# Kernel optimization log

Measured on AMD Instinct MI355X. Metric: run time of the kernel, lower is better.

The kernel has to match this reference:

```python
import jax, jax.numpy as jnp
import numpy as np

B, T, C = 4, 2048, 1024
H = 16
D = C // H  # head_dim = 64


def setup_inputs() -> dict:
    key = jax.random.key(0)
    k1, k2, k3 = jax.random.split(key, 3)
    x = jax.random.normal(k1, (B, T, C), dtype=jnp.float32)
    # torch Linear weights are [out_features, in_features]; scale like default init
    W_qkv = jax.random.normal(k2, (3 * C, C), dtype=jnp.float32) * (1.0 / np.sqrt(C))
    W_proj = jax.random.normal(k3, (C, C), dtype=jnp.float32) * (1.0 / np.sqrt(C))
    return {"x": x, "W_qkv": W_qkv, "W_proj": W_proj}


def reference(x, W_qkv, W_proj):
    # qkv projection: x @ W_qkv.T -> (B,T,3C), split into q,k,v
    qkv = jnp.einsum('btc,oc->bto', x, W_qkv)
    q, k, v = jnp.split(qkv, 3, axis=-1)
    # reshape to (B,H,T,D)
    q = q.reshape(B, T, H, D).transpose(0, 2, 1, 3)
    k = k.reshape(B, T, H, D).transpose(0, 2, 1, 3)
    v = v.reshape(B, T, H, D).transpose(0, 2, 1, 3)
    scale = jnp.sqrt(jnp.float32(D))
    # explicit (B,H,T,T) scores, as in the original module
    attn = jnp.einsum('bhqd,bhkd->bhqk', q, k) / scale
    causal = jnp.tril(jnp.ones((T, T), dtype=bool))
    attn = jnp.where(causal, attn, -jnp.inf)
    attn = jax.nn.softmax(attn, axis=-1)
    out = jnp.einsum('bhqk,bhkd->bhqd', attn, v)
    out = out.transpose(0, 2, 1, 3).reshape(B, T, C)
    return jnp.einsum('btc,oc->bto', out, W_proj)
```

## Files before the change

kernel.cpp:

```cpp
#include <hip/hip_runtime.h>

typedef __attribute__((ext_vector_type(8))) short short8;
typedef __attribute__((ext_vector_type(4))) float f32x4;
typedef __attribute__((ext_vector_type(16))) float f32x16;
typedef __attribute__((ext_vector_type(4))) unsigned int u32x4;

#define AS1(p) ((const __attribute__((address_space(1))) void*)(p))
#define AS3(p) ((__attribute__((address_space(3))) void*)(p))

#define B_ 4
#define T_ 2048
#define C_ 1024
#define H_ 16
#define D_ 64
#define M_ (B_*T_)

#define MFIX 16.0f

__device__ __forceinline__ unsigned short f2bf(float f) {
  union { float f; unsigned u; } v; v.f = f;
  return (unsigned short)((v.u + 0x7fffu + ((v.u >> 16) & 1u)) >> 16);
}

__device__ __forceinline__ unsigned cvt_pk_bf16(float lo, float hi2) {
  unsigned r;
  asm("v_cvt_pk_bf16_f32 %0, %1, %2" : "=v"(r) : "v"(lo), "v"(hi2));
  return r;
}

__device__ __forceinline__ float exp2_fast(float x) {
  return __builtin_amdgcn_exp2f(x);
}

__global__ void cast_f32_bf16(const float* __restrict__ in, unsigned short* __restrict__ out, int n) {
  int i = (blockIdx.x * blockDim.x + threadIdx.x) * 4;
  int stride = gridDim.x * blockDim.x * 4;
  for (; i < n; i += stride) {
    float4 f = *reinterpret_cast<const float4*>(in + i);
    ushort4 o;
    o.x = f2bf(f.x); o.y = f2bf(f.y); o.z = f2bf(f.z); o.w = f2bf(f.w);
    *reinterpret_cast<ushort4*>(out + i) = o;
  }
}

__global__ __launch_bounds__(512, 2) void gemm256_qkv(
    const unsigned short* __restrict__ A, const unsigned short* __restrict__ Bt,
    int M, int N, int K,
    unsigned short* __restrict__ qb, unsigned short* __restrict__ kb,
    unsigned short* __restrict__ vtb) {
  __shared__ unsigned short Ls[2][2][2][128 * 64];
  const int tid = threadIdx.x;
  const int lane = tid & 63;
  const int wid = tid >> 6;
  const int wm = wid >> 2;
  const int wn = wid & 3;
  const int lr = lane & 15, lg = lane >> 4;
  const int ntb_cnt = N >> 8;
  const int nwg = gridDim.x;
  const int cpx = nwg >> 3;
  const int wg = (blockIdx.x & 7) * cpx + (blockIdx.x >> 3);
  const int mt = wg / ntb_cnt, ntb = wg % ntb_cnt;
  const int m0 = mt << 8, n0 = ntb << 8;

  f32x4 acc[8][4];
  #pragma unroll
  for (int i = 0; i < 8; i++)
    #pragma unroll
    for (int j = 0; j < 4; j++) acc[i][j] = (f32x4){0.f, 0.f, 0.f, 0.f};

  const int wbase16 = (tid & ~63) * 16;

  auto stage = [&](int buf, int mat, int half, int k0) {
    const unsigned short* srcbase = (mat == 0) ? (A  + (size_t)(m0 + half * 128) * K)
                                               : (Bt + (size_t)(n0 + half * 128) * K);
    char* ldsbase = (char*)&Ls[buf][mat][half][0];
    #pragma unroll
    for (int i = 0; i < 2; i++) {
      int s = i * 512 + tid;
      int row = s >> 3;
      int src = ((s & 7) * 16) ^ ((row & 7) << 4);
      const unsigned short* g = srcbase + (size_t)row * K + k0 + (src >> 1);
      char* l = ldsbase + i * 8192 + wbase16;
      __builtin_amdgcn_global_load_lds(AS1(g), AS3(l), 16, 0, 0);
    }
  };

  const int ktiles = K >> 6;
  stage(0, 0, 0, 0); stage(0, 0, 1, 0); stage(0, 1, 0, 0); stage(0, 1, 1, 0);

  for (int t = 0; t < ktiles; ++t) {
    const int cur = t & 1;
    const int nk0 = (t + 1) << 6;
    const bool more = (t + 1 < ktiles);
    short8 bfrag[4][2];

    #pragma unroll
    for (int p = 0; p < 4; p++) {
      if (more) stage(cur ^ 1, p >> 1, p & 1, nk0);
      if (p == 0) {
        if (more) asm volatile("s_waitcnt vmcnt(2)" ::: "memory");
        else      asm volatile("s_waitcnt vmcnt(0)" ::: "memory");
      }
      __builtin_amdgcn_sched_barrier(0);
      __builtin_amdgcn_s_barrier();
      __builtin_amdgcn_sched_barrier(0);

      if (p == 0) {
        #pragma unroll
        for (int ni = 0; ni < 4; ni++)
          #pragma unroll
          for (int ks = 0; ks < 2; ks++) {
            const int rih = (wn & 1) * 64 + ni * 16 + lr;
            bfrag[ni][ks] = *reinterpret_cast<const short8*>(
                (const char*)&Ls[cur][1][wn >> 1][0] + rih * 128 +
                ((ks * 64 + lg * 16) ^ ((lr & 7) << 4)));
          }
      }
      short8 af[2][2];
      #pragma unroll
      for (int m2 = 0; m2 < 2; m2++)
        #pragma unroll
        for (int ks = 0; ks < 2; ks++) {
          const int rih = (2 * p + m2) * 16 + lr;
          af[m2][ks] = *reinterpret_cast<const short8*>(
              (const char*)&Ls[cur][0][wm][0] + rih * 128 +
              ((ks * 64 + lg * 16) ^ ((lr & 7) << 4)));
        }

      __builtin_amdgcn_s_setprio(1);
      #pragma unroll
      for (int m2 = 0; m2 < 2; m2++)
        #pragma unroll
        for (int ni = 0; ni < 4; ni++)
          #pragma unroll
          for (int ks = 0; ks < 2; ks++)
            acc[2 * p + m2][ni] = __builtin_amdgcn_mfma_f32_16x16x32_bf16(
                af[m2][ks], bfrag[ni][ks], acc[2 * p + m2][ni], 0, 0, 0);
      __builtin_amdgcn_s_setprio(0);
      __builtin_amdgcn_sched_barrier(0);
      __builtin_amdgcn_s_barrier();
    }
  }

  #pragma unroll
  for (int mi = 0; mi < 8; mi++) {
    #pragma unroll
    for (int ni = 0; ni < 4; ni++) {
      #pragma unroll
      for (int r = 0; r < 4; r++) {
        int row = m0 + wm * 128 + mi * 16 + lg * 4 + r;
        int col = n0 + wn * 64 + ni * 16 + lr;
        float v = acc[mi][ni][r];
        int which = col >> 10;
        int c = col & 1023;
        int h = c >> 6, d = c & 63;
        int b = row >> 11, t2 = row & 2047;
        if (which == 0) {
          qb[(((size_t)(b * H_ + h)) * T_ + t2) * D_ + d] = f2bf(v * 0.18033688f);
        } else if (which == 1) {
          kb[(((size_t)(b * H_ + h)) * T_ + t2) * D_ + d] = f2bf(v);
        } else {
          vtb[(((size_t)(b * H_ + h)) * D_ + d) * T_ + t2] = f2bf(v);
        }
      }
    }
  }
}

__global__ __launch_bounds__(256) void gemm_bt(
    const unsigned short* __restrict__ A, const unsigned short* __restrict__ Bt,
    float* __restrict__ Cout, int M, int N, int K) {
  __shared__ unsigned short As[2][128 * 32];
  __shared__ unsigned short Bs[2][128 * 32];
  const int tid = threadIdx.x;
  const int lane = tid & 63;
  const int w = tid >> 6;
  const int wr = w >> 1, wc = w & 1;
  const int lr = lane & 15, lg = lane >> 4;
  const int ntiles = N >> 7;
  const int nwg = gridDim.x;
  const int cpx = nwg >> 3;
  const int wg = (blockIdx.x & 7) * cpx + (blockIdx.x >> 3);
  const int mt = wg / ntiles, nt = wg % ntiles;
  const int m0 = mt << 7, n0 = nt << 7;

  f32x4 acc[4][4];
  #pragma unroll
  for (int i = 0; i < 4; i++)
    #pragma unroll
    for (int j = 0; j < 4; j++) acc[i][j] = (f32x4){0.f, 0.f, 0.f, 0.f};

  const int wbase = tid & ~63;

  auto stage = [&](int buf, int k0) {
    #pragma unroll
    for (int t = 0; t < 2; t++) {
      int slot = t * 256 + tid;
      int row = slot >> 2, kg = slot & 3;
      const unsigned short* ga = A + (size_t)(m0 + row) * K + k0 + kg * 8;
      char* la = (char*)As[buf] + (size_t)(t * 256 + wbase) * 16;
      __builtin_amdgcn_global_load_lds(AS1(ga), AS3(la), 16, 0, 0);
      const unsigned short* gb = Bt + (size_t)(n0 + row) * K + k0 + kg * 8;
      char* lb = (char*)Bs[buf] + (size_t)(t * 256 + wbase) * 16;
      __builtin_amdgcn_global_load_lds(AS1(gb), AS3(lb), 16, 0, 0);
    }
  };

  const int nIter = K >> 5;
  stage(0, 0);
  __syncthreads();

  for (int it = 0; it < nIter; ++it) {
    const int cur = it & 1;
    if (it + 1 < nIter) stage(cur ^ 1, (it + 1) << 5);

    short8 af[4], bf[4];
    #pragma unroll
    for (int i = 0; i < 4; i++) {
      af[i] = *reinterpret_cast<const short8*>(&As[cur][(wr * 64 + i * 16 + lr) * 32 + lg * 8]);
      bf[i] = *reinterpret_cast<const short8*>(&Bs[cur][(wc * 64 + i * 16 + lr) * 32 + lg * 8]);
    }
    #pragma unroll
    for (int i = 0; i < 4; i++)
      #pragma unroll
      for (int j = 0; j < 4; j++)
        acc[i][j] = __builtin_amdgcn_mfma_f32_16x16x32_bf16(af[i], bf[j], acc[i][j], 0, 0, 0);

    __syncthreads();
  }

  #pragma unroll
  for (int i = 0; i < 4; i++)
    #pragma unroll
    for (int j = 0; j < 4; j++)
      #pragma unroll
      for (int r = 0; r < 4; r++) {
        int row = m0 + wr * 64 + i * 16 + lg * 4 + r;
        int col = n0 + wc * 64 + j * 16 + lr;
        Cout[(size_t)row * N + col] = acc[i][j][r];
      }
}

__global__ __launch_bounds__(128, 2) void attn_fwd(
    const unsigned short* __restrict__ qb, const unsigned short* __restrict__ kb,
    const unsigned short* __restrict__ vtb, unsigned short* __restrict__ ob) {
  __shared__ unsigned short Kl[2 * 64 * 64];
  const int tid = threadIdx.x;
  const int lane = tid & 63;
  const int w = tid >> 6;
  const int q31 = lane & 31;
  const int hi = lane >> 5;

  const int bid = blockIdx.x;
  const int bh = (bid & 7) * 8 + ((bid >> 3) & 7);
  const int qt = 15 - (bid >> 6);
  const int qb0 = qt << 7;
  const int b = bh >> 4, h = bh & 15;

  const unsigned short* Q  = qb  + (size_t)bh * T_ * D_;
  const unsigned short* Kp = kb  + (size_t)bh * T_ * D_;
  const unsigned short* Vt = vtb + (size_t)bh * D_ * T_;

  const int qloA = qb0 + w * 64;
  const int qloB = qloA + 32;
  const int qgA = qloA + q31;
  const int qgB = qloB + q31;

  short8 qfA[4], qfB[4];
  #pragma unroll
  for (int ch = 0; ch < 4; ch++) {
    qfA[ch] = *reinterpret_cast<const short8*>(Q + qgA * D_ + ch * 16 + hi * 8);
    qfB[ch] = *reinterpret_cast<const short8*>(Q + qgB * D_ + ch * 16 + hi * 8);
  }

  f32x16 accA0, accA1, accB0, accB1;
  #pragma unroll
  for (int r = 0; r < 16; r++) { accA0[r] = 0.f; accA1[r] = 0.f; accB0[r] = 0.f; accB1[r] = 0.f; }
  float lA = 0.f, lB = 0.f;

  auto stage = [&](int buf, int k0) {
    #pragma unroll
    for (int sh = 0; sh < 4; sh++) {
      int s = sh * 128 + tid;
      int row = s >> 3;
      int xlin = (s & 7) * 16;
      int src = xlin ^ ((row & 7) << 4);
      const unsigned short* g = Kp + (k0 + row) * D_ + (src >> 1);
      char* l = (char*)Kl + buf * 8192 + (size_t)(sh * 128 + (tid & ~63)) * 16;
      __builtin_amdgcn_global_load_lds(AS1(g), AS3(l), 16, 0, 0);
    }
  };

  const int nt = qb0 / 64 + 2;
  stage(0, 0);
  __syncthreads();

  for (int t = 0; t < nt; t++) {
    const int k0 = t * 64;
    if (t + 1 < nt) stage((t + 1) & 1, k0 + 64);

    if (k0 <= qloA + 63) {
      short8 vf[2][4];
      #pragma unroll
      for (int ds = 0; ds < 2; ds++)
        #pragma unroll
        for (int kk = 0; kk < 4; kk++)
          vf[ds][kk] = *reinterpret_cast<const short8*>(
              Vt + (ds * 32 + q31) * T_ + k0 + kk * 16 + hi * 8);
      __builtin_amdgcn_sched_barrier(0);

      const char* kbase = (const char*)Kl + (t & 1) * 8192;

      f32x16 sA0, sA1, sB0, sB1;
      #pragma unroll
      for (int r = 0; r < 16; r++) { sA0[r] = 0.f; sA1[r] = 0.f; sB0[r] = 0.f; sB1[r] = 0.f; }
      __builtin_amdgcn_s_setprio(1);
      #pragma unroll
      for (int kc = 0; kc < 2; kc++) {
        const int row = kc * 32 + q31;
        const int sw = (row & 7) << 4;
        #pragma unroll
        for (int ch = 0; ch < 4; ch++) {
          short8 kf = *reinterpret_cast<const short8*>(kbase + row * 128 + ((ch * 32 + hi * 16) ^ sw));
          if (kc == 0) {
            sA0 = __builtin_amdgcn_mfma_f32_32x32x16_bf16(kf, qfA[ch], sA0, 0, 0, 0);
            sB0 = __builtin_amdgcn_mfma_f32_32x32x16_bf16(kf, qfB[ch], sB0, 0, 0, 0);
          } else {
            sA1 = __builtin_amdgcn_mfma_f32_32x32x16_bf16(kf, qfA[ch], sA1, 0, 0, 0);
            sB1 = __builtin_amdgcn_mfma_f32_32x32x16_bf16(kf, qfB[ch], sB1, 0, 0, 0);
          }
        }
      }
      __builtin_amdgcn_s_setprio(0);

      if (k0 + 63 > qloA) {
        #pragma unroll
        for (int r = 0; r < 16; r++) {
          const int kl = (r & 3) + 8 * (r >> 2) + 4 * hi;
          if (k0 + kl > qgA)      sA0[r] = -INFINITY;
          if (k0 + 32 + kl > qgA) sA1[r] = -INFINITY;
        }
      }
      if (k0 + 63 > qloB) {
        #pragma unroll
        for (int r = 0; r < 16; r++) {
          const int kl = (r & 3) + 8 * (r >> 2) + 4 * hi;
          if (k0 + kl > qgB)      sB0[r] = -INFINITY;
          if (k0 + 32 + kl > qgB) sB1[r] = -INFINITY;
        }
      }

      #pragma unroll
      for (int r = 0; r < 16; r++) {
        sA0[r] = exp2_fast(sA0[r] - MFIX); sA1[r] = exp2_fast(sA1[r] - MFIX);
        sB0[r] = exp2_fast(sB0[r] - MFIX); sB1[r] = exp2_fast(sB1[r] - MFIX);
      }
      {
        float tsA[8], tsB[8];
        #pragma unroll
        for (int r = 0; r < 8; r++) {
          tsA[r] = (sA0[r] + sA0[r + 8]) + (sA1[r] + sA1[r + 8]);
          tsB[r] = (sB0[r] + sB0[r + 8]) + (sB1[r] + sB1[r + 8]);
        }
        #pragma unroll
        for (int off = 4; off > 0; off >>= 1)
          #pragma unroll
          for (int r = 0; r < off; r++) { tsA[r] += tsA[r + off]; tsB[r] += tsB[r + off]; }
        lA += tsA[0];
        lB += tsB[0];
      }

      #pragma unroll
      for (int kc = 0; kc < 2; kc++) {
        unsigned w8A[8], rw8A[8], w8B[8], rw8B[8];
        #pragma unroll
        for (int j = 0; j < 8; j++) {
          float aA  = (kc == 0) ? sA0[2 * j] : sA1[2 * j];
          float bA  = (kc == 0) ? sA0[2 * j + 1] : sA1[2 * j + 1];
          w8A[j] = cvt_pk_bf16(aA, bA);
          float aB  = (kc == 0) ? sB0[2 * j] : sB1[2 * j];
          float bB  = (kc == 0) ? sB0[2 * j + 1] : sB1[2 * j + 1];
          w8B[j] = cvt_pk_bf16(aB, bB);
        }
        #pragma unroll
        for (int j = 0; j < 8; j++) {
          rw8A[j] = (unsigned)__shfl_xor((int)w8A[j], 32);
          rw8B[j] = (unsigned)__shfl_xor((int)w8B[j], 32);
        }

        __builtin_amdgcn_s_setprio(1);
        #pragma unroll
        for (int ks = 0; ks < 2; ks++) {
          unsigned a0 = hi ? rw8A[4 * ks + 2] : w8A[4 * ks + 0];
          unsigned a1 = hi ? rw8A[4 * ks + 3] : w8A[4 * ks + 1];
          unsigned a2 = hi ? w8A[4 * ks + 2]  : rw8A[4 * ks + 0];
          unsigned a3 = hi ? w8A[4 * ks + 3]  : rw8A[4 * ks + 1];
          u32x4 pwA = {a0, a1, a2, a3};
          unsigned b0 = hi ? rw8B[4 * ks + 2] : w8B[4 * ks + 0];
          unsigned b1 = hi ? rw8B[4 * ks + 3] : w8B[4 * ks + 1];
          unsigned b2 = hi ? w8B[4 * ks + 2]  : rw8B[4 * ks + 0];
          unsigned b3 = hi ? w8B[4 * ks + 3]  : rw8B[4 * ks + 1];
          u32x4 pwB = {b0, b1, b2, b3};
          union { u32x4 u; short8 s; } cvA, cvB;
          cvA.u = pwA; cvB.u = pwB;
          const int kk = kc * 2 + ks;
          #pragma unroll
          for (int ds = 0; ds < 2; ds++) {
            if (ds == 0) {
              accA0 = __builtin_amdgcn_mfma_f32_32x32x16_bf16(vf[0][kk], cvA.s, accA0, 0, 0, 0);
              accB0 = __builtin_amdgcn_mfma_f32_32x32x16_bf16(vf[0][kk], cvB.s, accB0, 0, 0, 0);
            } else {
              accA1 = __builtin_amdgcn_mfma_f32_32x32x16_bf16(vf[1][kk], cvA.s, accA1, 0, 0, 0);
              accB1 = __builtin_amdgcn_mfma_f32_32x32x16_bf16(vf[1][kk], cvB.s, accB1, 0, 0, 0);
            }
          }
        }
        __builtin_amdgcn_s_setprio(0);
      }
    }
    __syncthreads();
  }

  lA += __shfl_xor(lA, 32);
  lB += __shfl_xor(lB, 32);

  {
    const float invA = 1.f / lA;
    unsigned short* orow = ob + ((size_t)(b * T_ + qgA)) * C_ + h * D_;
    #pragma unroll
    for (int ds = 0; ds < 2; ds++) {
      #pragma unroll
      for (int g = 0; g < 4; g++) {
        ushort4 o4;
        if (ds == 0) {
          o4.x = f2bf(accA0[4 * g + 0] * invA); o4.y = f2bf(accA0[4 * g + 1] * invA);
          o4.z = f2bf(accA0[4 * g + 2] * invA); o4.w = f2bf(accA0[4 * g + 3] * invA);
        } else {
          o4.x = f2bf(accA1[4 * g + 0] * invA); o4.y = f2bf(accA1[4 * g + 1] * invA);
          o4.z = f2bf(accA1[4 * g + 2] * invA); o4.w = f2bf(accA1[4 * g + 3] * invA);
        }
        *reinterpret_cast<ushort4*>(orow + ds * 32 + 8 * g + 4 * hi) = o4;
      }
    }
  }
  {
    const float invB = 1.f / lB;
    unsigned short* orow = ob + ((size_t)(b * T_ + qgB)) * C_ + h * D_;
    #pragma unroll
    for (int ds = 0; ds < 2; ds++) {
      #pragma unroll
      for (int g = 0; g < 4; g++) {
        ushort4 o4;
        if (ds == 0) {
          o4.x = f2bf(accB0[4 * g + 0] * invB); o4.y = f2bf(accB0[4 * g + 1] * invB);
          o4.z = f2bf(accB0[4 * g + 2] * invB); o4.w = f2bf(accB0[4 * g + 3] * invB);
        } else {
          o4.x = f2bf(accB1[4 * g + 0] * invB); o4.y = f2bf(accB1[4 * g + 1] * invB);
          o4.z = f2bf(accB1[4 * g + 2] * invB); o4.w = f2bf(accB1[4 * g + 3] * invB);
        }
        *reinterpret_cast<ushort4*>(orow + ds * 32 + 8 * g + 4 * hi) = o4;
      }
    }
  }
}

extern "C" void kernel_launch(void* const* d_in, const int* in_sizes, int n_in,
                              void* d_out, int out_size, void* d_ws, size_t ws_size,
                              hipStream_t stream) {
  const float* x = (const float*)d_in[0];
  const float* W_qkv = (const float*)d_in[1];
  const float* W_proj = (const float*)d_in[2];
  float* out = (float*)d_out;

  char* ws = (char*)d_ws;
  unsigned short* xb     = (unsigned short*)(ws);
  unsigned short* wqkvb  = (unsigned short*)(ws + 16777216);
  unsigned short* wprojb = (unsigned short*)(ws + 23068672);
  unsigned short* qb     = (unsigned short*)(ws + 25165824);
  unsigned short* kb     = (unsigned short*)(ws + 41943040);
  unsigned short* vtb    = (unsigned short*)(ws + 58720256);
  unsigned short* ob     = xb;

  const int nx = M_ * C_;
  const int nwqkv = 3 * C_ * C_;
  const int nwproj = C_ * C_;

  cast_f32_bf16<<<2048, 256, 0, stream>>>(x, xb, nx);
  cast_f32_bf16<<<2048, 256, 0, stream>>>(W_qkv, wqkvb, nwqkv);
  cast_f32_bf16<<<1024, 256, 0, stream>>>(W_proj, wprojb, nwproj);

  gemm256_qkv<<<(M_ / 256) * (3 * C_ / 256), 512, 0, stream>>>(
      xb, wqkvb, M_, 3 * C_, C_, qb, kb, vtb);

  attn_fwd<<<B_ * H_ * (T_ / 128), 128, 0, stream>>>(qb, kb, vtb, ob);

  gemm_bt<<<(M_ / 128) * (C_ / 128), 256, 0, stream>>>(
      ob, wprojb, out, M_, C_, C_);
}
```

Measured before the change: 205.2 us.

## Split attention into single-wave blocks of 64 query rows with waitcnt-based pipelining

The attention kernel now launches one 64-thread wavefront per 64-row query tile, doubling the grid and removing the two-wave block. With a single wave, __syncthreads is replaced by explicit s_waitcnt vmcnt on the async K-to-LDS staging, and the per-wave causal skip branch is dropped because every tile iterates only up to its diagonal. This removes block-level barriers and the idle tail of the second wave, at the cost of K tiles no longer being shared across two waves through LDS. Occupancy also changes through the launch bounds and per-block LDS use.

```diff
diff --git a/kernel.cpp b/kernel.cpp
--- a/kernel.cpp
+++ b/kernel.cpp
@@ -241,30 +241,26 @@
       }
 }
 
-__global__ __launch_bounds__(128, 2) void attn_fwd(
+__global__ __launch_bounds__(64, 1) void attn_fwd(
     const unsigned short* __restrict__ qb, const unsigned short* __restrict__ kb,
     const unsigned short* __restrict__ vtb, unsigned short* __restrict__ ob) {
   __shared__ unsigned short Kl[2 * 64 * 64];
-  const int tid = threadIdx.x;
-  const int lane = tid & 63;
-  const int w = tid >> 6;
+  const int lane = threadIdx.x;
   const int q31 = lane & 31;
   const int hi = lane >> 5;
 
   const int bid = blockIdx.x;
   const int bh = (bid & 7) * 8 + ((bid >> 3) & 7);
-  const int qt = 15 - (bid >> 6);
-  const int qb0 = qt << 7;
+  const int qt = 31 - (bid >> 6);
+  const int qb0 = qt << 6;
   const int b = bh >> 4, h = bh & 15;
 
   const unsigned short* Q  = qb  + (size_t)bh * T_ * D_;
   const unsigned short* Kp = kb  + (size_t)bh * T_ * D_;
   const unsigned short* Vt = vtb + (size_t)bh * D_ * T_;
 
-  const int qloA = qb0 + w * 64;
-  const int qloB = qloA + 32;
-  const int qgA = qloA + q31;
-  const int qgB = qloB + q31;
+  const int qgA = qb0 + q31;
+  const int qgB = qb0 + 32 + q31;
 
   short8 qfA[4], qfB[4];
   #pragma unroll
@@ -280,145 +276,140 @@
 
   auto stage = [&](int buf, int k0) {
     #pragma unroll
-    for (int sh = 0; sh < 4; sh++) {
-      int s = sh * 128 + tid;
+    for (int sh = 0; sh < 8; sh++) {
+      int s = sh * 64 + lane;
       int row = s >> 3;
-      int xlin = (s & 7) * 16;
-      int src = xlin ^ ((row & 7) << 4);
+      int src = ((s & 7) * 16) ^ ((row & 7) << 4);
       const unsigned short* g = Kp + (k0 + row) * D_ + (src >> 1);
-      char* l = (char*)Kl + buf * 8192 + (size_t)(sh * 128 + (tid & ~63)) * 16;
+      char* l = (char*)Kl + buf * 8192 + sh * 1024;
       __builtin_amdgcn_global_load_lds(AS1(g), AS3(l), 16, 0, 0);
     }
   };
 
-  const int nt = qb0 / 64 + 2;
+  const int nt = qt + 1;
   stage(0, 0);
-  __syncthreads();
 
   for (int t = 0; t < nt; t++) {
     const int k0 = t * 64;
-    if (t + 1 < nt) stage((t + 1) & 1, k0 + 64);
-
-    if (k0 <= qloA + 63) {
-      short8 vf[2][4];
-      #pragma unroll
-      for (int ds = 0; ds < 2; ds++)
+    if (t + 1 < nt) {
+      stage((t + 1) & 1, k0 + 64);
+      asm volatile("s_waitcnt vmcnt(8)" ::: "memory");
+    } else {
+      asm volatile("s_waitcnt vmcnt(0)" ::: "memory");
+    }
+    __builtin_amdgcn_sched_barrier(0);
+
+    short8 vf[2][4];
+    #pragma unroll
+    for (int ds = 0; ds < 2; ds++)
+      #pragma unroll
+      for (int kk = 0; kk < 4; kk++)
+        vf[ds][kk] = *reinterpret_cast<const short8*>(
+            Vt + (ds * 32 + q31) * T_ + k0 + kk * 16 + hi * 8);
+    __builtin_amdgcn_sched_barrier(0);
+
+    const char* kbase = (const char*)Kl + (t & 1) * 8192;
+
+    f32x16 sA0, sA1, sB0, sB1;
+    #pragma unroll
+    for (int r = 0; r < 16; r++) { sA0[r] = 0.f; sA1[r] = 0.f; sB0[r] = 0.f; sB1[r] = 0.f; }
+    __builtin_amdgcn_s_setprio(1);
+    #pragma unroll
+    for (int kc = 0; kc < 2; kc++) {
+      const int row = kc * 32 + q31;
+      const int sw = (row & 7) << 4;
+      #pragma unroll
+      for (int ch = 0; ch < 4; ch++) {
+        short8 kf = *reinterpret_cast<const short8*>(kbase + row * 128 + ((ch * 32 + hi * 16) ^ sw));
+        if (kc == 0) {
+          sA0 = __builtin_amdgcn_mfma_f32_32x32x16_bf16(kf, qfA[ch], sA0, 0, 0, 0);
+          sB0 = __builtin_amdgcn_mfma_f32_32x32x16_bf16(kf, qfB[ch], sB0, 0, 0, 0);
+        } else {
+          sA1 = __builtin_amdgcn_mfma_f32_32x32x16_bf16(kf, qfA[ch], sA1, 0, 0, 0);
+          sB1 = __builtin_amdgcn_mfma_f32_32x32x16_bf16(kf, qfB[ch], sB1, 0, 0, 0);
+        }
+      }
+    }
+    __builtin_amdgcn_s_setprio(0);
+
+    if (t == nt - 1) {
+      #pragma unroll
+      for (int r = 0; r < 16; r++) {
+        const int kl = (r & 3) + 8 * (r >> 2) + 4 * hi;
+        if (k0 + kl > qgA)      sA0[r] = -INFINITY;
+        if (k0 + 32 + kl > qgA) sA1[r] = -INFINITY;
+        if (k0 + kl > qgB)      sB0[r] = -INFINITY;
+        if (k0 + 32 + kl > qgB) sB1[r] = -INFINITY;
+      }
+    }
+
+    #pragma unroll
+    for (int r = 0; r < 16; r++) {
+      sA0[r] = exp2_fast(sA0[r] - MFIX); sA1[r] = exp2_fast(sA1[r] - MFIX);
+      sB0[r] = exp2_fast(sB0[r] - MFIX); sB1[r] = exp2_fast(sB1[r] - MFIX);
+    }
+    {
+      float tsA[8], tsB[8];
+      #pragma unroll
+      for (int r = 0; r < 8; r++) {
+        tsA[r] = (sA0[r] + sA0[r + 8]) + (sA1[r] + sA1[r + 8]);
+        tsB[r] = (sB0[r] + sB0[r + 8]) + (sB1[r] + sB1[r + 8]);
+      }
+      #pragma unroll
+      for (int off = 4; off > 0; off >>= 1)
         #pragma unroll
-        for (int kk = 0; kk < 4; kk++)
-          vf[ds][kk] = *reinterpret_cast<const short8*>(
-              Vt + (ds * 32 + q31) * T_ + k0 + kk * 16 + hi * 8);
-      __builtin_amdgcn_sched_barrier(0);
-
-      const char* kbase = (const char*)Kl + (t & 1) * 8192;
-
-      f32x16 sA0, sA1, sB0, sB1;
-      #pragma unroll
-      for (int r = 0; r < 16; r++) { sA0[r] = 0.f; sA1[r] = 0.f; sB0[r] = 0.f; sB1[r] = 0.f; }
+        for (int r = 0; r < off; r++) { tsA[r] += tsA[r + off]; tsB[r] += tsB[r + off]; }
+      lA += tsA[0];
+      lB += tsB[0];
+    }
+
+    #pragma unroll
+    for (int kc = 0; kc < 2; kc++) {
+      unsigned w8A[8], rw8A[8], w8B[8], rw8B[8];
+      #pragma unroll
+      for (int j = 0; j < 8; j++) {
+        float aA  = (kc == 0) ? sA0[2 * j] : sA1[2 * j];
+        float bA  = (kc == 0) ? sA0[2 * j + 1] : sA1[2 * j + 1];
+        w8A[j] = cvt_pk_bf16(aA, bA);
+        float aB  = (kc == 0) ? sB0[2 * j] : sB1[2 * j];
+        float bB  = (kc == 0) ? sB0[2 * j + 1] : sB1[2 * j + 1];
+        w8B[j] = cvt_pk_bf16(aB, bB);
+      }
+      #pragma unroll
+      for (int j = 0; j < 8; j++) {
+        rw8A[j] = (unsigned)__shfl_xor((int)w8A[j], 32);
+        rw8B[j] = (unsigned)__shfl_xor((int)w8B[j], 32);
+      }
+
       __builtin_amdgcn_s_setprio(1);
       #pragma unroll
-      for (int kc = 0; kc < 2; kc++) {
-        const int row = kc * 32 + q31;
-        const int sw = (row & 7) << 4;
+      for (int ks = 0; ks < 2; ks++) {
+        unsigned a0 = hi ? rw8A[4 * ks + 2] : w8A[4 * ks + 0];
+        unsigned a1 = hi ? rw8A[4 * ks + 3] : w8A[4 * ks + 1];
+        unsigned a2 = hi ? w8A[4 * ks + 2]  : rw8A[4 * ks + 0];
+        unsigned a3 = hi ? w8A[4 * ks + 3]  : rw8A[4 * ks + 1];
+        u32x4 pwA = {a0, a1, a2, a3};
+        unsigned b0 = hi ? rw8B[4 * ks + 2] : w8B[4 * ks + 0];
+        unsigned b1 = hi ? rw8B[4 * ks + 3] : w8B[4 * ks + 1];
+        unsigned b2 = hi ? w8B[4 * ks + 2]  : rw8B[4 * ks + 0];
+        unsigned b3 = hi ? w8B[4 * ks + 3]  : rw8B[4 * ks + 1];
+        u32x4 pwB = {b0, b1, b2, b3};
+        union { u32x4 u; short8 s; } cvA, cvB;
+        cvA.u = pwA; cvB.u = pwB;
+        const int kk = kc * 2 + ks;
         #pragma unroll
-        for (int ch = 0; ch < 4; ch++) {
-          short8 kf = *reinterpret_cast<const short8*>(kbase + row * 128 + ((ch * 32 + hi * 16) ^ sw));
-          if (kc == 0) {
-            sA0 = __builtin_amdgcn_mfma_f32_32x32x16_bf16(kf, qfA[ch], sA0, 0, 0, 0);
-            sB0 = __builtin_amdgcn_mfma_f32_32x32x16_bf16(kf, qfB[ch], sB0, 0, 0, 0);
+        for (int ds = 0; ds < 2; ds++) {
+          if (ds == 0) {
+            accA0 = __builtin_amdgcn_mfma_f32_32x32x16_bf16(vf[0][kk], cvA.s, accA0, 0, 0, 0);
+            accB0 = __builtin_amdgcn_mfma_f32_32x32x16_bf16(vf[0][kk], cvB.s, accB0, 0, 0, 0);
           } else {
-            sA1 = __builtin_amdgcn_mfma_f32_32x32x16_bf16(kf, qfA[ch], sA1, 0, 0, 0);
-            sB1 = __builtin_amdgcn_mfma_f32_32x32x16_bf16(kf, qfB[ch], sB1, 0, 0, 0);
+            accA1 = __builtin_amdgcn_mfma_f32_32x32x16_bf16(vf[1][kk], cvA.s, accA1, 0, 0, 0);
+            accB1 = __builtin_amdgcn_mfma_f32_32x32x16_bf16(vf[1][kk], cvB.s, accB1, 0, 0, 0);
           }
         }
       }
       __builtin_amdgcn_s_setprio(0);
-
-      if (k0 + 63 > qloA) {
-        #pragma unroll
-        for (int r = 0; r < 16; r++) {
-          const int kl = (r & 3) + 8 * (r >> 2) + 4 * hi;
-          if (k0 + kl > qgA)      sA0[r] = -INFINITY;
-          if (k0 + 32 + kl > qgA) sA1[r] = -INFINITY;
-        }
-      }
-      if (k0 + 63 > qloB) {
-        #pragma unroll
-        for (int r = 0; r < 16; r++) {
-          const int kl = (r & 3) + 8 * (r >> 2) + 4 * hi;
-          if (k0 + kl > qgB)      sB0[r] = -INFINITY;
-          if (k0 + 32 + kl > qgB) sB1[r] = -INFINITY;
-        }
-      }
-
-      #pragma unroll
-      for (int r = 0; r < 16; r++) {
-        sA0[r] = exp2_fast(sA0[r] - MFIX); sA1[r] = exp2_fast(sA1[r] - MFIX);
-        sB0[r] = exp2_fast(sB0[r] - MFIX); sB1[r] = exp2_fast(sB1[r] - MFIX);
-      }
-      {
-        float tsA[8], tsB[8];
-        #pragma unroll
-        for (int r = 0; r < 8; r++) {
-          tsA[r] = (sA0[r] + sA0[r + 8]) + (sA1[r] + sA1[r + 8]);
-          tsB[r] = (sB0[r] + sB0[r + 8]) + (sB1[r] + sB1[r + 8]);
-        }
-        #pragma unroll
-        for (int off = 4; off > 0; off >>= 1)
-          #pragma unroll
-          for (int r = 0; r < off; r++) { tsA[r] += tsA[r + off]; tsB[r] += tsB[r + off]; }
-        lA += tsA[0];
-        lB += tsB[0];
-      }
-
-      #pragma unroll
-      for (int kc = 0; kc < 2; kc++) {
-        unsigned w8A[8], rw8A[8], w8B[8], rw8B[8];
-        #pragma unroll
-        for (int j = 0; j < 8; j++) {
-          float aA  = (kc == 0) ? sA0[2 * j] : sA1[2 * j];
-          float bA  = (kc == 0) ? sA0[2 * j + 1] : sA1[2 * j + 1];
-          w8A[j] = cvt_pk_bf16(aA, bA);
-          float aB  = (kc == 0) ? sB0[2 * j] : sB1[2 * j];
-          float bB  = (kc == 0) ? sB0[2 * j + 1] : sB1[2 * j + 1];
-          w8B[j] = cvt_pk_bf16(aB, bB);
-        }
-        #pragma unroll
-        for (int j = 0; j < 8; j++) {
-          rw8A[j] = (unsigned)__shfl_xor((int)w8A[j], 32);
-          rw8B[j] = (unsigned)__shfl_xor((int)w8B[j], 32);
-        }
-
-        __builtin_amdgcn_s_setprio(1);
-        #pragma unroll
-        for (int ks = 0; ks < 2; ks++) {
-          unsigned a0 = hi ? rw8A[4 * ks + 2] : w8A[4 * ks + 0];
-          unsigned a1 = hi ? rw8A[4 * ks + 3] : w8A[4 * ks + 1];
-          unsigned a2 = hi ? w8A[4 * ks + 2]  : rw8A[4 * ks + 0];
-          unsigned a3 = hi ? w8A[4 * ks + 3]  : rw8A[4 * ks + 1];
-          u32x4 pwA = {a0, a1, a2, a3};
-          unsigned b0 = hi ? rw8B[4 * ks + 2] : w8B[4 * ks + 0];
-          unsigned b1 = hi ? rw8B[4 * ks + 3] : w8B[4 * ks + 1];
-          unsigned b2 = hi ? w8B[4 * ks + 2]  : rw8B[4 * ks + 0];
-          unsigned b3 = hi ? w8B[4 * ks + 3]  : rw8B[4 * ks + 1];
-          u32x4 pwB = {b0, b1, b2, b3};
-          union { u32x4 u; short8 s; } cvA, cvB;
-          cvA.u = pwA; cvB.u = pwB;
-          const int kk = kc * 2 + ks;
-          #pragma unroll
-          for (int ds = 0; ds < 2; ds++) {
-            if (ds == 0) {
-              accA0 = __builtin_amdgcn_mfma_f32_32x32x16_bf16(vf[0][kk], cvA.s, accA0, 0, 0, 0);
-              accB0 = __builtin_amdgcn_mfma_f32_32x32x16_bf16(vf[0][kk], cvB.s, accB0, 0, 0, 0);
-            } else {
-              accA1 = __builtin_amdgcn_mfma_f32_32x32x16_bf16(vf[1][kk], cvA.s, accA1, 0, 0, 0);
-              accB1 = __builtin_amdgcn_mfma_f32_32x32x16_bf16(vf[1][kk], cvB.s, accB1, 0, 0, 0);
-            }
-          }
-        }
-        __builtin_amdgcn_s_setprio(0);
-      }
-    }
-    __syncthreads();
+    }
   }
 
   lA += __shfl_xor(lA, 32);
@@ -492,7 +483,7 @@
   gemm256_qkv<<<(M_ / 256) * (3 * C_ / 256), 512, 0, stream>>>(
       xb, wqkvb, M_, 3 * C_, C_, qb, kb, vtb);
 
-  attn_fwd<<<B_ * H_ * (T_ / 128), 128, 0, stream>>>(qb, kb, vtb, ob);
+  attn_fwd<<<B_ * H_ * (T_ / 64), 64, 0, stream>>>(qb, kb, vtb, ob);
 
   gemm_bt<<<(M_ / 128) * (C_ / 128), 256, 0, stream>>>(
       ob, wprojb, out, M_, C_, C_);
```

After: 207.6 us. Within noise of the previous version (+1.2%).
